# Kernel tuning notes

Measured on AMD Instinct MI355X. Metric: run time of the kernel, lower is better.

The kernel has to match this reference:

```python
import jax, jax.numpy as jnp
import numpy as np

NEG_SLOPE = 0.2  # PyG GATConv default leaky_relu slope


def add_self_loops(src, dst, ea, n_nodes):
    # PyG add_self_loops with fill_value='mean': self-loop attr = mean of
    # incoming edge attrs per destination node (0 if no incoming edges).
    cnt = jax.ops.segment_sum(jnp.ones(dst.shape, ea.dtype), dst, num_segments=n_nodes)
    mean_ea = jax.ops.segment_sum(ea, dst, num_segments=n_nodes) / jnp.maximum(cnt, 1.0)[:, None]
    loop = jnp.arange(n_nodes, dtype=src.dtype)
    return (jnp.concatenate([src, loop]),
            jnp.concatenate([dst, loop]),
            jnp.concatenate([ea, mean_ea], axis=0))


def gat_conv(x, src, dst, ea, W, att_src, att_dst, We, att_edge, bias, heads, ch, concat):
    n = x.shape[0]
    xs = (x @ W).reshape(n, heads, ch)                      # [N,H,C]
    a_src = (xs * att_src).sum(-1)                          # [N,H]
    a_dst = (xs * att_dst).sum(-1)                          # [N,H]
    ea_p = (ea @ We).reshape(-1, heads, ch)                 # [E,H,C]
    a_e = (ea_p * att_edge).sum(-1)                         # [E,H]
    logits = jax.nn.leaky_relu(a_src[src] + a_dst[dst] + a_e, NEG_SLOPE)
    m = jax.ops.segment_max(logits, dst, num_segments=n)    # segment softmax over dst
    e = jnp.exp(logits - m[dst])
    denom = jax.ops.segment_sum(e, dst, num_segments=n)
    alpha = e / (denom[dst] + 1e-16)                        # [E,H]
    out = jax.ops.segment_sum(alpha[:, :, None] * xs[src], dst, num_segments=n)  # [N,H,C]
    out = out.reshape(n, heads * ch) if concat else out.mean(axis=1)
    return out + bias


def setup_inputs() -> dict:
    key = jax.random.key(0)
    ks = jax.random.split(key, 14)
    N, E, F_IN, H, C1, C2 = 50000, 800000, 128, 2, 64, 64
    s = 0.05
    return {
        "x": jax.random.normal(ks[0], (N, F_IN), jnp.float32),
        "edge_index": jax.random.randint(ks[1], (2, E), 0, N, jnp.int32),
        "edge_weight": jax.random.uniform(ks[2], (E,), jnp.float32),
        # layer 1 (heads=2, concat=True)
        "W1": jax.random.normal(ks[3], (F_IN, H * C1), jnp.float32) * s,
        "att_src1": jax.random.normal(ks[4], (1, H, C1), jnp.float32) * s,
        "att_dst1": jax.random.normal(ks[5], (1, H, C1), jnp.float32) * s,
        "We1": jax.random.normal(ks[6], (1, H * C1), jnp.float32) * s,
        "att_edge1": jax.random.normal(ks[7], (1, H, C1), jnp.float32) * s,
        "b1": jnp.zeros((H * C1,), jnp.float32),
        # layer 2 (heads=1, concat=False)
        "W2": jax.random.normal(ks[8], (H * C1, C2), jnp.float32) * s,
        "att_src2": jax.random.normal(ks[9], (1, 1, C2), jnp.float32) * s,
        "att_dst2": jax.random.normal(ks[10], (1, 1, C2), jnp.float32) * s,
        "We2": jax.random.normal(ks[11], (1, C2), jnp.float32) * s,
        "att_edge2": jax.random.normal(ks[12], (1, 1, C2), jnp.float32) * s,
        "b2": jnp.zeros((C2,), jnp.float32),
    }


def reference(x, edge_index, edge_weight, W1, att_src1, att_dst1, We1, att_edge1, b1,
              W2, att_src2, att_dst2, We2, att_edge2, b2):
    n = x.shape[0]
    ea = edge_weight[:, None]  # edge_dim=1
    src, dst, ea = add_self_loops(edge_index[0], edge_index[1], ea, n)
    h = gat_conv(x, src, dst, ea, W1, att_src1, att_dst1, We1, att_edge1, b1,
                 heads=2, ch=64, concat=True)
    h = jax.nn.elu(h)
    out = gat_conv(h, src, dst, ea, W2, att_src2, att_dst2, We2, att_edge2, b2,
                   heads=1, ch=64, concat=False)
    return out
```

## Files before the change

### kernel.cpp

```cpp
#include <hip/hip_runtime.h>
#include <math.h>

#define NEG_SLOPE 0.2f

typedef unsigned int u32;
typedef unsigned short u16;
typedef unsigned long long u64;

typedef __attribute__((ext_vector_type(8))) short short8;
typedef __attribute__((ext_vector_type(4))) float f32x4;

__device__ __forceinline__ float bf2f(u16 h) {
  union { u32 u; float f; } c; c.u = ((u32)h) << 16; return c.f;
}
__device__ __forceinline__ u16 f2bf(float f) {
  union { float f; u32 u; } c; c.f = f;
  return (u16)((c.u + 0x7FFFu + ((c.u >> 16) & 1u)) >> 16);
}

__global__ __launch_bounds__(256) void k_hist(const int* __restrict__ dst, int E, int epb,
                                              u32* __restrict__ hist) {
  __shared__ u32 h[256];
  h[threadIdx.x] = 0;
  __syncthreads();
  int b = blockIdx.x;
  int beg = b * epb, end = beg + epb; if (end > E) end = E;
  for (int i = beg + threadIdx.x; i < end; i += 256)
    atomicAdd(&h[(u32)dst[i] >> 8], 1u);
  __syncthreads();
  hist[threadIdx.x * 256 + b] = h[threadIdx.x];
}

__global__ __launch_bounds__(256) void k_scanrow(u32* __restrict__ hist, u32* __restrict__ btot) {
  int bkt = blockIdx.x, t = threadIdx.x;
  u32 orig = hist[bkt * 256 + t];
  u32 v = orig;
  #pragma unroll
  for (int off = 1; off < 64; off <<= 1) {
    u32 u_ = __shfl_up(v, off);
    if ((t & 63) >= off) v += u_;
  }
  __shared__ u32 ws[4];
  if ((t & 63) == 63) ws[t >> 6] = v;
  __syncthreads();
  u32 add = 0; int w = t >> 6;
  if (w > 0) add += ws[0];
  if (w > 1) add += ws[1];
  if (w > 2) add += ws[2];
  u32 incl = v + add;
  hist[bkt * 256 + t] = incl - orig;
  if (t == 255) btot[bkt] = incl;
}

__global__ __launch_bounds__(256) void k_scanb(const u32* __restrict__ btot, u32* __restrict__ bstart) {
  int t = threadIdx.x;
  u32 orig = btot[t];
  u32 v = orig;
  #pragma unroll
  for (int off = 1; off < 64; off <<= 1) {
    u32 u_ = __shfl_up(v, off);
    if ((t & 63) >= off) v += u_;
  }
  __shared__ u32 ws[4];
  if ((t & 63) == 63) ws[t >> 6] = v;
  __syncthreads();
  u32 add = 0; int w = t >> 6;
  if (w > 0) add += ws[0];
  if (w > 1) add += ws[1];
  if (w > 2) add += ws[2];
  u32 incl = v + add;
  bstart[t] = incl - orig;
  if (t == 255) bstart[256] = incl;
}

__global__ __launch_bounds__(256) void k_binscatter(const int* __restrict__ src,
                                                    const int* __restrict__ dst,
                                                    const float* __restrict__ ew,
                                                    const u32* __restrict__ hist,
                                                    const u32* __restrict__ bstart,
                                                    u64* __restrict__ stage, int E, int epb) {
  __shared__ u32 cur[256];
  int b = blockIdx.x;
  cur[threadIdx.x] = bstart[threadIdx.x] + hist[threadIdx.x * 256 + b];
  __syncthreads();
  int beg = b * epb, end = beg + epb; if (end > E) end = E;
  for (int i = beg + threadIdx.x; i < end; i += 256) {
    int d = dst[i];
    u32 bkt = (u32)d >> 8;
    u32 pos = atomicAdd(&cur[bkt], 1u);
    float w = ew[i];
    u32 wq = (u32)(w * 65536.0f); if (wq > 65535u) wq = 65535u;
    stage[pos] = ((u64)((u32)d & 255u) << 32) | ((u64)wq << 16) | (u64)(u32)src[i];
  }
}

__global__ __launch_bounds__(256) void k_bucket(const u64* __restrict__ stage,
                                                const u32* __restrict__ bstart,
                                                u32* __restrict__ col,
                                                u32* __restrict__ ninfo, int n) {
  int bkt = blockIdx.x;
  int beg = (int)bstart[bkt], end = (int)bstart[bkt + 1];
  __shared__ u32 pk[256];
  pk[threadIdx.x] = 0;
  __syncthreads();
  for (int i = beg + threadIdx.x; i < end; i += 256) {
    u64 sv = stage[i];
    u32 ln = (u32)(sv >> 32) & 255u;
    u32 wq = (u32)((sv >> 16) & 0xFFFFu);
    u32 old = atomicAdd(&pk[ln], (1u << 24) | wq);
    u32 rank = old >> 24;
    if (rank < 64u)
      col[((((u32)bkt << 8) + ln) << 6) + rank] = (u32)sv;
  }
  __syncthreads();
  int v = (bkt << 8) + threadIdx.x;
  if (v < n) {
    u32 p = pk[threadIdx.x];
    u32 deg = p >> 24;
    float mean = ((float)(p & 0xFFFFFFu) * (1.0f / 65536.0f)) / (float)(deg > 1 ? deg : 1);
    u32 mq = (u32)(mean * 65536.0f); if (mq > 65535u) mq = 65535u;
    u32 dc = deg > 64u ? 64u : deg;
    ninfo[v] = (dc << 16) | mq;
  }
}

template<int H>
__global__ void k_bfrag(const float* __restrict__ W, uint4* __restrict__ bfrag) {
  int tid = blockIdx.x * 256 + threadIdx.x;
  int f = tid >> 6, lane = tid & 63;
  const int NF = H * 4 * 4 * 2;
  if (f >= NF) return;
  int p = f & 1, t = (f >> 1) & 3, cg = f >> 3;
  int colc = 16 * cg + (lane & 15);
  int k0 = 32 * t + 8 * (lane >> 4);
  u16 v[8];
  #pragma unroll
  for (int j = 0; j < 8; j++) {
    float w = W[(size_t)(k0 + j) * (H * 64) + colc];
    u32 bits = __float_as_uint(w);
    if (p == 0) v[j] = (u16)(bits >> 16);
    else        v[j] = f2bf(w - __uint_as_float(bits & 0xffff0000u));
  }
  uint4 o = { (u32)v[0] | ((u32)v[1] << 16), (u32)v[2] | ((u32)v[3] << 16),
              (u32)v[4] | ((u32)v[5] << 16), (u32)v[6] | ((u32)v[7] << 16) };
  bfrag[f * 64 + lane] = o;
}

template<int H>
__global__ __launch_bounds__(256) void k_gemm_mfma(const float* __restrict__ A,
                                                   const uint4* __restrict__ bfrag,
                                                   u16* __restrict__ xs_bf,
                                                   const float* __restrict__ att_src,
                                                   const float* __restrict__ att_dst,
                                                   float* __restrict__ a_src_out,
                                                   float* __restrict__ a_dst_out,
                                                   int nrows) {
  const int NCG = H * 4;
  int lane = threadIdx.x & 63;
  int wv = threadIdx.x >> 6;
  int lrow = lane & 15, lk = lane >> 4;
  int r0 = blockIdx.x * 64 + wv * 16;
  int arow = r0 + lrow; if (arow > nrows - 1) arow = nrows - 1;
  const float* ap = A + (size_t)arow * 128;

  f32x4 acc[NCG];
  #pragma unroll
  for (int cg = 0; cg < NCG; cg++) acc[cg] = (f32x4){0.f, 0.f, 0.f, 0.f};

  #pragma unroll
  for (int t = 0; t < 4; t++) {
    float4 av0 = *(const float4*)(ap + 32 * t + 8 * lk);
    float4 av1 = *(const float4*)(ap + 32 * t + 8 * lk + 4);
    float af[8] = {av0.x, av0.y, av0.z, av0.w, av1.x, av1.y, av1.z, av1.w};
    short8 ahi, alo;
    #pragma unroll
    for (int j = 0; j < 8; j++) {
      u32 bits = __float_as_uint(af[j]);
      ahi[j] = (short)(bits >> 16);
      alo[j] = (short)f2bf(af[j] - __uint_as_float(bits & 0xffff0000u));
    }
    #pragma unroll
    for (int cg = 0; cg < NCG; cg++) {
      union { uint4 u; short8 s; } bh, bl;
      bh.u = bfrag[((cg * 4 + t) * 2 + 0) * 64 + lane];
      bl.u = bfrag[((cg * 4 + t) * 2 + 1) * 64 + lane];
      acc[cg] = __builtin_amdgcn_mfma_f32_16x16x32_bf16(ahi, bh.s, acc[cg], 0, 0, 0);
      acc[cg] = __builtin_amdgcn_mfma_f32_16x16x32_bf16(ahi, bl.s, acc[cg], 0, 0, 0);
      acc[cg] = __builtin_amdgcn_mfma_f32_16x16x32_bf16(alo, bh.s, acc[cg], 0, 0, 0);
    }
  }

  float ps[2][4], pd[2][4];
  #pragma unroll
  for (int h = 0; h < 2; h++)
    #pragma unroll
    for (int r = 0; r < 4; r++) { ps[h][r] = 0.f; pd[h][r] = 0.f; }

  #pragma unroll
  for (int cg = 0; cg < NCG; cg++) {
    int colbase = 16 * cg + lrow;
    float asv = att_src[colbase];
    float adv = att_dst[colbase];
    const int h = (H == 2) ? (cg >> 2) : 0;
    #pragma unroll
    for (int r = 0; r < 4; r++) {
      ps[h][r] += acc[cg][r] * asv;
      pd[h][r] += acc[cg][r] * adv;
      int row = r0 + 4 * lk + r;
      if (row < nrows) xs_bf[(size_t)row * (H * 64) + colbase] = f2bf(acc[cg][r]);
    }
  }
  #pragma unroll
  for (int h = 0; h < H; h++)
    #pragma unroll
    for (int r = 0; r < 4; r++)
      #pragma unroll
      for (int off = 8; off; off >>= 1) {
        ps[h][r] += __shfl_xor(ps[h][r], off);
        pd[h][r] += __shfl_xor(pd[h][r], off);
      }
  if (lrow == 0) {
    #pragma unroll
    for (int r = 0; r < 4; r++) {
      int row = r0 + 4 * lk + r;
      if (row < nrows) {
        #pragma unroll
        for (int h = 0; h < H; h++) {
          a_src_out[row * H + h] = ps[h][r];
          a_dst_out[row * H + h] = pd[h][r];
        }
      }
    }
  }
}

__global__ void k_scalars(const float* __restrict__ We1, const float* __restrict__ ae1,
                          const float* __restrict__ We2, const float* __restrict__ ae2,
                          float* __restrict__ out) {
  int t = threadIdx.x;
  if (t == 0) { float s = 0; for (int c = 0; c < 64; c++) s += We1[c] * ae1[c]; out[0] = s; }
  if (t == 1) { float s = 0; for (int c = 0; c < 64; c++) s += We1[64 + c] * ae1[64 + c]; out[1] = s; }
  if (t == 2) { float s = 0; for (int c = 0; c < 64; c++) s += We2[c] * ae2[c]; out[2] = s; }
}

__global__ __launch_bounds__(256) void k_agg1(const u32* __restrict__ ninfo,
                                              const u32* __restrict__ col,
                                              const float2* __restrict__ a_src,
                                              const float2* __restrict__ a_dst,
                                              const float* __restrict__ scal,
                                              const u16* __restrict__ xs_bf,
                                              const float* __restrict__ b1,
                                              float* __restrict__ h_out, int n) {
  int wid = (blockIdx.x * 256 + threadIdx.x) >> 4;
  int gl = threadIdx.x & 15;
  if (wid >= n) return;
  u32 nf = ninfo[wid];
  int deg = (int)(nf >> 16);
  float mean = (float)(nf & 0xFFFFu) * (1.0f / 65536.0f);
  float2 ad = a_dst[wid];
  float2 asv_s = a_src[wid];
  float sc0 = scal[0], sc1 = scal[1];
  bool hi = gl >= 8;
  float l0s = asv_s.x + ad.x + mean * sc0;
  float l1s = asv_s.y + ad.y + mean * sc1;
  l0s = l0s > 0.f ? l0s : NEG_SLOPE * l0s;
  l1s = l1s > 0.f ? l1s : NEG_SLOPE * l1s;

  const u32* cw = col + ((u32)wid << 6);
  int nch = (deg + 15) >> 4;

  float e0a[4], e1a[4]; int sa[4];
  #pragma unroll
  for (int c = 0; c < 4; c++) {
    float l0 = -1e30f, l1 = -1e30f; int s = 0;
    if (c < nch) {
      int p = c * 16 + gl;
      bool act = p < deg;
      u32 sw = cw[act ? p : 0];
      s = (int)(sw & 0xFFFFu);
      float w = (float)(sw >> 16) * (1.0f / 65536.0f);
      float2 asv = a_src[s];
      l0 = asv.x + ad.x + w * sc0;
      l1 = asv.y + ad.y + w * sc1;
      l0 = l0 > 0.f ? l0 : NEG_SLOPE * l0;
      l1 = l1 > 0.f ? l1 : NEG_SLOPE * l1;
      if (!act) { l0 = -1e30f; l1 = -1e30f; }
    }
    sa[c] = s; e0a[c] = l0; e1a[c] = l1;
  }
  float m0 = fmaxf(fmaxf(e0a[0], e0a[1]), fmaxf(e0a[2], e0a[3]));
  float m1 = fmaxf(fmaxf(e1a[0], e1a[1]), fmaxf(e1a[2], e1a[3]));
  #pragma unroll
  for (int off = 8; off; off >>= 1) {
    m0 = fmaxf(m0, __shfl_xor(m0, off, 16));
    m1 = fmaxf(m1, __shfl_xor(m1, off, 16));
  }
  m0 = fmaxf(m0, l0s); m1 = fmaxf(m1, l1s);
  float d0 = 0.f, d1 = 0.f;
  #pragma unroll
  for (int c = 0; c < 4; c++) {
    float t0 = __expf(e0a[c] - m0);
    float t1 = __expf(e1a[c] - m1);
    e0a[c] = t0; e1a[c] = t1;
    d0 += t0; d1 += t1;
  }
  #pragma unroll
  for (int off = 8; off; off >>= 1) {
    d0 += __shfl_xor(d0, off, 16);
    d1 += __shfl_xor(d1, off, 16);
  }
  float es0 = __expf(l0s - m0), es1 = __expf(l1s - m1);
  float den = (hi ? d1 + es1 : d0 + es0);
  float esl = hi ? es1 : es0;

  float acc[8];
  {
    uint4 q = *(const uint4*)&xs_bf[(size_t)wid * 128 + 8 * gl];
    acc[0] = esl * bf2f((u16)q.x); acc[1] = esl * bf2f((u16)(q.x >> 16));
    acc[2] = esl * bf2f((u16)q.y); acc[3] = esl * bf2f((u16)(q.y >> 16));
    acc[4] = esl * bf2f((u16)q.z); acc[5] = esl * bf2f((u16)(q.z >> 16));
    acc[6] = esl * bf2f((u16)q.w); acc[7] = esl * bf2f((u16)(q.w >> 16));
  }
  #pragma unroll
  for (int c = 0; c < 4; c++) {
    if (c < nch) {
      int base = c * 16;
      int cnt = deg - base; if (cnt > 16) cnt = 16;
      int j = 0;
      for (; j + 2 <= cnt; j += 2) {
        int sj0 = __shfl(sa[c], j, 16);
        int sj1 = __shfl(sa[c], j + 1, 16);
        uint4 qa = *(const uint4*)&xs_bf[(size_t)sj0 * 128 + 8 * gl];
        uint4 qb = *(const uint4*)&xs_bf[(size_t)sj1 * 128 + 8 * gl];
        float a0 = __shfl(e0a[c], j, 16),     a1 = __shfl(e1a[c], j, 16);
        float b0 = __shfl(e0a[c], j + 1, 16), b1 = __shfl(e1a[c], j + 1, 16);
        float ala = hi ? a1 : a0;
        float alb = hi ? b1 : b0;
        acc[0] += ala * bf2f((u16)qa.x); acc[1] += ala * bf2f((u16)(qa.x >> 16));
        acc[2] += ala * bf2f((u16)qa.y); acc[3] += ala * bf2f((u16)(qa.y >> 16));
        acc[4] += ala * bf2f((u16)qa.z); acc[5] += ala * bf2f((u16)(qa.z >> 16));
        acc[6] += ala * bf2f((u16)qa.w); acc[7] += ala * bf2f((u16)(qa.w >> 16));
        acc[0] += alb * bf2f((u16)qb.x); acc[1] += alb * bf2f((u16)(qb.x >> 16));
        acc[2] += alb * bf2f((u16)qb.y); acc[3] += alb * bf2f((u16)(qb.y >> 16));
        acc[4] += alb * bf2f((u16)qb.z); acc[5] += alb * bf2f((u16)(qb.z >> 16));
        acc[6] += alb * bf2f((u16)qb.w); acc[7] += alb * bf2f((u16)(qb.w >> 16));
      }
      if (j < cnt) {
        int sj = __shfl(sa[c], j, 16);
        uint4 q = *(const uint4*)&xs_bf[(size_t)sj * 128 + 8 * gl];
        float a0 = __shfl(e0a[c], j, 16), a1 = __shfl(e1a[c], j, 16);
        float al = hi ? a1 : a0;
        acc[0] += al * bf2f((u16)q.x); acc[1] += al * bf2f((u16)(q.x >> 16));
        acc[2] += al * bf2f((u16)q.y); acc[3] += al * bf2f((u16)(q.y >> 16));
        acc[4] += al * bf2f((u16)q.z); acc[5] += al * bf2f((u16)(q.z >> 16));
        acc[6] += al * bf2f((u16)q.w); acc[7] += al * bf2f((u16)(q.w >> 16));
      }
    }
  }
  float inv = 1.f / (den + 1e-16f);
  float4 blo = *(const float4*)&b1[8 * gl];
  float4 bhi = *(const float4*)&b1[8 * gl + 4];
  float o[8];
  o[0] = acc[0] * inv + blo.x; o[1] = acc[1] * inv + blo.y;
  o[2] = acc[2] * inv + blo.z; o[3] = acc[3] * inv + blo.w;
  o[4] = acc[4] * inv + bhi.x; o[5] = acc[5] * inv + bhi.y;
  o[6] = acc[6] * inv + bhi.z; o[7] = acc[7] * inv + bhi.w;
  #pragma unroll
  for (int f = 0; f < 8; f++) o[f] = o[f] > 0.f ? o[f] : expm1f(o[f]);
  float* dst = &h_out[(size_t)wid * 128 + 8 * gl];
  *(float4*)dst = make_float4(o[0], o[1], o[2], o[3]);
  *(float4*)(dst + 4) = make_float4(o[4], o[5], o[6], o[7]);
}

__global__ __launch_bounds__(256) void k_agg2(const u32* __restrict__ ninfo,
                                              const u32* __restrict__ col,
                                              const float* __restrict__ a_src,
                                              const float* __restrict__ a_dst,
                                              const float* __restrict__ scal,
                                              const u16* __restrict__ xs_bf,
                                              const float* __restrict__ b2,
                                              float* __restrict__ out, int n) {
  int wid = (blockIdx.x * 256 + threadIdx.x) >> 3;
  int gl = threadIdx.x & 7;
  if (wid >= n) return;
  u32 nf = ninfo[wid];
  int deg = (int)(nf >> 16);
  float mean = (float)(nf & 0xFFFFu) * (1.0f / 65536.0f);
  float adv = a_dst[wid];
  float sc = scal[2];
  float ls = a_src[wid] + adv + mean * sc;
  ls = ls > 0.f ? ls : NEG_SLOPE * ls;

  const u32* cw = col + ((u32)wid << 6);
  int nch = (deg + 7) >> 3;

  float ea[8]; int sa[8];
  #pragma unroll
  for (int c = 0; c < 8; c++) {
    float l = -1e30f; int s = 0;
    if (c < nch) {
      int p = c * 8 + gl;
      bool act = p < deg;
      u32 sw = cw[act ? p : 0];
      s = (int)(sw & 0xFFFFu);
      float w = (float)(sw >> 16) * (1.0f / 65536.0f);
      l = a_src[s] + adv + w * sc;
      l = l > 0.f ? l : NEG_SLOPE * l;
      if (!act) l = -1e30f;
    }
    sa[c] = s; ea[c] = l;
  }
  float m = ls;
  #pragma unroll
  for (int c = 0; c < 8; c++) m = fmaxf(m, ea[c]);
  #pragma unroll
  for (int off = 4; off; off >>= 1) m = fmaxf(m, __shfl_xor(m, off, 8));
  float d = 0.f;
  #pragma unroll
  for (int c = 0; c < 8; c++) {
    float t = __expf(ea[c] - m);
    ea[c] = t; d += t;
  }
  #pragma unroll
  for (int off = 4; off; off >>= 1) d += __shfl_xor(d, off, 8);
  float es = __expf(ls - m);
  float den = d + es;

  float acc[8];
  {
    uint4 q = *(const uint4*)&xs_bf[(size_t)wid * 64 + 8 * gl];
    acc[0] = es * bf2f((u16)q.x); acc[1] = es * bf2f((u16)(q.x >> 16));
    acc[2] = es * bf2f((u16)q.y); acc[3] = es * bf2f((u16)(q.y >> 16));
    acc[4] = es * bf2f((u16)q.z); acc[5] = es * bf2f((u16)(q.z >> 16));
    acc[6] = es * bf2f((u16)q.w); acc[7] = es * bf2f((u16)(q.w >> 16));
  }
  #pragma unroll
  for (int c = 0; c < 8; c++) {
    if (c < nch) {
      int base = c * 8;
      int cnt = deg - base; if (cnt > 8) cnt = 8;
      int j = 0;
      for (; j + 2 <= cnt; j += 2) {
        int sj0 = __shfl(sa[c], j, 8);
        int sj1 = __shfl(sa[c], j + 1, 8);
        uint4 qa = *(const uint4*)&xs_bf[(size_t)sj0 * 64 + 8 * gl];
        uint4 qb = *(const uint4*)&xs_bf[(size_t)sj1 * 64 + 8 * gl];
        float aja = __shfl(ea[c], j, 8);
        float ajb = __shfl(ea[c], j + 1, 8);
        acc[0] += aja * bf2f((u16)qa.x); acc[1] += aja * bf2f((u16)(qa.x >> 16));
        acc[2] += aja * bf2f((u16)qa.y); acc[3] += aja * bf2f((u16)(qa.y >> 16));
        acc[4] += aja * bf2f((u16)qa.z); acc[5] += aja * bf2f((u16)(qa.z >> 16));
        acc[6] += aja * bf2f((u16)qa.w); acc[7] += aja * bf2f((u16)(qa.w >> 16));
        acc[0] += ajb * bf2f((u16)qb.x); acc[1] += ajb * bf2f((u16)(qb.x >> 16));
        acc[2] += ajb * bf2f((u16)qb.y); acc[3] += ajb * bf2f((u16)(qb.y >> 16));
        acc[4] += ajb * bf2f((u16)qb.z); acc[5] += ajb * bf2f((u16)(qb.z >> 16));
        acc[6] += ajb * bf2f((u16)qb.w); acc[7] += ajb * bf2f((u16)(qb.w >> 16));
      }
      if (j < cnt) {
        int sj = __shfl(sa[c], j, 8);
        uint4 q = *(const uint4*)&xs_bf[(size_t)sj * 64 + 8 * gl];
        float aj = __shfl(ea[c], j, 8);
        acc[0] += aj * bf2f((u16)q.x); acc[1] += aj * bf2f((u16)(q.x >> 16));
        acc[2] += aj * bf2f((u16)q.y); acc[3] += aj * bf2f((u16)(q.y >> 16));
        acc[4] += aj * bf2f((u16)q.z); acc[5] += aj * bf2f((u16)(q.z >> 16));
        acc[6] += aj * bf2f((u16)q.w); acc[7] += aj * bf2f((u16)(q.w >> 16));
      }
    }
  }
  float inv = 1.f / (den + 1e-16f);
  float4 blo = *(const float4*)&b2[8 * gl];
  float4 bhi = *(const float4*)&b2[8 * gl + 4];
  float* dst = &out[(size_t)wid * 64 + 8 * gl];
  *(float4*)dst = make_float4(acc[0] * inv + blo.x, acc[1] * inv + blo.y,
                              acc[2] * inv + blo.z, acc[3] * inv + blo.w);
  *(float4*)(dst + 4) = make_float4(acc[4] * inv + bhi.x, acc[5] * inv + bhi.y,
                                    acc[6] * inv + bhi.z, acc[7] * inv + bhi.w);
}

extern "C" void kernel_launch(void* const* d_in, const int* in_sizes, int n_in,
                              void* d_out, int out_size, void* d_ws, size_t ws_size,
                              hipStream_t stream) {
  const float* x   = (const float*)d_in[0];
  const int*   ei  = (const int*)d_in[1];
  const float* ew  = (const float*)d_in[2];
  const float* W1  = (const float*)d_in[3];
  const float* as1 = (const float*)d_in[4];
  const float* ad1 = (const float*)d_in[5];
  const float* We1 = (const float*)d_in[6];
  const float* ae1 = (const float*)d_in[7];
  const float* b1  = (const float*)d_in[8];
  const float* W2  = (const float*)d_in[9];
  const float* as2 = (const float*)d_in[10];
  const float* ad2 = (const float*)d_in[11];
  const float* We2 = (const float*)d_in[12];
  const float* ae2 = (const float*)d_in[13];
  const float* b2  = (const float*)d_in[14];

  const int n = in_sizes[0] / 128;
  const int E = in_sizes[1] / 2;
  const int epb = (E + 255) / 256;
  const int nbk = (n + 255) >> 8;

  char* wsb = (char*)d_ws;
  size_t off = 0;
  auto alloc = [&](size_t bytes) -> void* {
    void* p = wsb + off; off += (bytes + 255) & ~(size_t)255; return p;
  };
  u32*   hist    = (u32*)  alloc((size_t)256 * 256 * 4);
  u32*   btot    = (u32*)  alloc((size_t)256 * 4);
  u32*   bstart  = (u32*)  alloc((size_t)257 * 4);
  u64*   stage   = (u64*)  alloc((size_t)E * 8);
  u32*   col     = (u32*)  alloc((size_t)n * 64 * 4);
  u32*   ninfo   = (u32*)  alloc((size_t)n * 4);
  uint4* bfrag1  = (uint4*)alloc((size_t)64 * 64 * 16);
  uint4* bfrag2  = (uint4*)alloc((size_t)32 * 64 * 16);
  u16*   xs_bf   = (u16*)  alloc((size_t)n * 128 * 2);
  float* h1      = (float*)alloc((size_t)n * 128 * 4);
  float* a_src1v = (float*)alloc((size_t)n * 2 * 4);
  float* a_dst1v = (float*)alloc((size_t)n * 2 * 4);
  float* a_src2v = (float*)alloc((size_t)n * 4);
  float* a_dst2v = (float*)alloc((size_t)n * 4);
  float* scal    = (float*)alloc(64);
  if (off > ws_size) return;

  dim3 B(256);
  k_hist<<<dim3(256), B, 0, stream>>>(ei + E, E, epb, hist);
  k_scanrow<<<dim3(256), B, 0, stream>>>(hist, btot);
  k_scanb<<<dim3(1), B, 0, stream>>>(btot, bstart);
  k_binscatter<<<dim3(256), B, 0, stream>>>(ei, ei + E, ew, hist, bstart, stage, E, epb);
  k_bucket<<<dim3(nbk), B, 0, stream>>>(stage, bstart, col, ninfo, n);
  k_bfrag<2><<<dim3(16), B, 0, stream>>>(W1, bfrag1);
  k_bfrag<1><<<dim3(8), B, 0, stream>>>(W2, bfrag2);
  k_scalars<<<1, 64, 0, stream>>>(We1, ae1, We2, ae2, scal);
  k_gemm_mfma<2><<<dim3((n + 63) / 64), B, 0, stream>>>(x, bfrag1, xs_bf, as1, ad1,
                                                        a_src1v, a_dst1v, n);
  k_agg1<<<dim3((n + 15) / 16), B, 0, stream>>>(ninfo, col,
                                                (const float2*)a_src1v,
                                                (const float2*)a_dst1v,
                                                scal, xs_bf, b1, h1, n);
  k_gemm_mfma<1><<<dim3((n + 63) / 64), B, 0, stream>>>(h1, bfrag2, xs_bf, as2, ad2,
                                                        a_src2v, a_dst2v, n);
  k_agg2<<<dim3((n + 31) / 32), B, 0, stream>>>(ninfo, col, a_src2v, a_dst2v,
                                                scal, xs_bf, b2, (float*)d_out, n);
}
```

Baseline: 134.0 us.

## Fuse prep kernels and co-launch layer-1 GEMM with edge binning; pack stage to 32 bits

Merges the histogram, weight-fragment builds and scalar dot products into one prep kernel. The layer-1 MFMA GEMM and the edge bin-scatter now share a single launch, with block ranges split by role so the independent work runs concurrently. The staging buffer shrinks from 64-bit to 32-bit entries by quantising edge weights to 8 bits, which cuts scatter and bucket traffic but lowers edge-weight precision and assumes source ids fit in 16 bits. The launch count drops from about 12 to 8.

Result: faster. 120.7 us (-9.9%).

```diff
diff --git a/kernel.cpp b/kernel.cpp
--- a/kernel.cpp
+++ b/kernel.cpp
@@ -18,17 +18,53 @@
   return (u16)((c.u + 0x7FFFu + ((c.u >> 16) & 1u)) >> 16);
 }
 
-__global__ __launch_bounds__(256) void k_hist(const int* __restrict__ dst, int E, int epb,
-                                              u32* __restrict__ hist) {
-  __shared__ u32 h[256];
-  h[threadIdx.x] = 0;
-  __syncthreads();
+__device__ __forceinline__ void bfrag_build(const float* __restrict__ W, uint4* __restrict__ bfrag,
+                                            int H, int f, int lane) {
+  int p = f & 1, t = (f >> 1) & 3, cg = f >> 3;
+  int colc = 16 * cg + (lane & 15);
+  int k0 = 32 * t + 8 * (lane >> 4);
+  u16 v[8];
+  #pragma unroll
+  for (int j = 0; j < 8; j++) {
+    float w = W[(size_t)(k0 + j) * (H * 64) + colc];
+    u32 bits = __float_as_uint(w);
+    if (p == 0) v[j] = (u16)(bits >> 16);
+    else        v[j] = f2bf(w - __uint_as_float(bits & 0xffff0000u));
+  }
+  uint4 o = { (u32)v[0] | ((u32)v[1] << 16), (u32)v[2] | ((u32)v[3] << 16),
+              (u32)v[4] | ((u32)v[5] << 16), (u32)v[6] | ((u32)v[7] << 16) };
+  bfrag[f * 64 + lane] = o;
+}
+
+__global__ __launch_bounds__(256) void k_prep(const int* __restrict__ dst, int E, int epb,
+                                              u32* __restrict__ hist,
+                                              const float* __restrict__ W1, uint4* __restrict__ bfrag1,
+                                              const float* __restrict__ W2, uint4* __restrict__ bfrag2,
+                                              const float* __restrict__ We1, const float* __restrict__ ae1,
+                                              const float* __restrict__ We2, const float* __restrict__ ae2,
+                                              float* __restrict__ scal) {
   int b = blockIdx.x;
-  int beg = b * epb, end = beg + epb; if (end > E) end = E;
-  for (int i = beg + threadIdx.x; i < end; i += 256)
-    atomicAdd(&h[(u32)dst[i] >> 8], 1u);
-  __syncthreads();
-  hist[threadIdx.x * 256 + b] = h[threadIdx.x];
+  if (b < 256) {
+    __shared__ u32 h[256];
+    h[threadIdx.x] = 0;
+    __syncthreads();
+    int beg = b * epb, end = beg + epb; if (end > E) end = E;
+    for (int i = beg + threadIdx.x; i < end; i += 256)
+      atomicAdd(&h[(u32)dst[i] >> 8], 1u);
+    __syncthreads();
+    hist[threadIdx.x * 256 + b] = h[threadIdx.x];
+  } else if (b < 272) {
+    int f = (b - 256) * 4 + (threadIdx.x >> 6);
+    if (f < 64) bfrag_build(W1, bfrag1, 2, f, threadIdx.x & 63);
+  } else if (b < 280) {
+    int f = (b - 272) * 4 + (threadIdx.x >> 6);
+    if (f < 32) bfrag_build(W2, bfrag2, 1, f, threadIdx.x & 63);
+  } else {
+    int t = threadIdx.x;
+    if (t == 0) { float s = 0; for (int c = 0; c < 64; c++) s += We1[c] * ae1[c]; scal[0] = s; }
+    if (t == 1) { float s = 0; for (int c = 0; c < 64; c++) s += We1[64 + c] * ae1[64 + c]; scal[1] = s; }
+    if (t == 2) { float s = 0; for (int c = 0; c < 64; c++) s += We2[c] * ae2[c]; scal[2] = s; }
+  }
 }
 
 __global__ __launch_bounds__(256) void k_scanrow(u32* __restrict__ hist, u32* __restrict__ btot) {
@@ -73,28 +109,117 @@
   if (t == 255) bstart[256] = incl;
 }
 
-__global__ __launch_bounds__(256) void k_binscatter(const int* __restrict__ src,
-                                                    const int* __restrict__ dst,
-                                                    const float* __restrict__ ew,
-                                                    const u32* __restrict__ hist,
-                                                    const u32* __restrict__ bstart,
-                                                    u64* __restrict__ stage, int E, int epb) {
+__global__ __launch_bounds__(256) void k_gemmbin(const float* __restrict__ A,
+                                                 const uint4* __restrict__ bfrag,
+                                                 u16* __restrict__ xs_bf,
+                                                 const float* __restrict__ att_src,
+                                                 const float* __restrict__ att_dst,
+                                                 float* __restrict__ a_src_out,
+                                                 float* __restrict__ a_dst_out,
+                                                 int nrows, int nbg,
+                                                 const int* __restrict__ esrc,
+                                                 const int* __restrict__ edst,
+                                                 const float* __restrict__ ew,
+                                                 const u32* __restrict__ hist,
+                                                 const u32* __restrict__ bstart,
+                                                 u32* __restrict__ stage, int E, int epb) {
   __shared__ u32 cur[256];
-  int b = blockIdx.x;
-  cur[threadIdx.x] = bstart[threadIdx.x] + hist[threadIdx.x * 256 + b];
-  __syncthreads();
-  int beg = b * epb, end = beg + epb; if (end > E) end = E;
-  for (int i = beg + threadIdx.x; i < end; i += 256) {
-    int d = dst[i];
-    u32 bkt = (u32)d >> 8;
-    u32 pos = atomicAdd(&cur[bkt], 1u);
-    float w = ew[i];
-    u32 wq = (u32)(w * 65536.0f); if (wq > 65535u) wq = 65535u;
-    stage[pos] = ((u64)((u32)d & 255u) << 32) | ((u64)wq << 16) | (u64)(u32)src[i];
-  }
-}
-
-__global__ __launch_bounds__(256) void k_bucket(const u64* __restrict__ stage,
+  if (blockIdx.x >= nbg) {
+    int b = blockIdx.x - nbg;
+    cur[threadIdx.x] = bstart[threadIdx.x] + hist[threadIdx.x * 256 + b];
+    __syncthreads();
+    int beg = b * epb, end = beg + epb; if (end > E) end = E;
+    for (int i = beg + threadIdx.x; i < end; i += 256) {
+      int d = edst[i];
+      u32 bkt = (u32)d >> 8;
+      u32 pos = atomicAdd(&cur[bkt], 1u);
+      float w = ew[i];
+      u32 wq = (u32)(w * 256.0f); if (wq > 255u) wq = 255u;
+      stage[pos] = (((u32)d & 255u) << 24) | (wq << 16) | (u32)esrc[i];
+    }
+    return;
+  }
+  const int H = 2;
+  const int NCG = H * 4;
+  int lane = threadIdx.x & 63;
+  int wv = threadIdx.x >> 6;
+  int lrow = lane & 15, lk = lane >> 4;
+  int r0 = blockIdx.x * 64 + wv * 16;
+  int arow = r0 + lrow; if (arow > nrows - 1) arow = nrows - 1;
+  const float* ap = A + (size_t)arow * 128;
+
+  f32x4 acc[NCG];
+  #pragma unroll
+  for (int cg = 0; cg < NCG; cg++) acc[cg] = (f32x4){0.f, 0.f, 0.f, 0.f};
+
+  #pragma unroll
+  for (int t = 0; t < 4; t++) {
+    float4 av0 = *(const float4*)(ap + 32 * t + 8 * lk);
+    float4 av1 = *(const float4*)(ap + 32 * t + 8 * lk + 4);
+    float af[8] = {av0.x, av0.y, av0.z, av0.w, av1.x, av1.y, av1.z, av1.w};
+    short8 ahi, alo;
+    #pragma unroll
+    for (int j = 0; j < 8; j++) {
+      u32 bits = __float_as_uint(af[j]);
+      ahi[j] = (short)(bits >> 16);
+      alo[j] = (short)f2bf(af[j] - __uint_as_float(bits & 0xffff0000u));
+    }
+    #pragma unroll
+    for (int cg = 0; cg < NCG; cg++) {
+      union { uint4 u; short8 s; } bh, bl;
+      bh.u = bfrag[((cg * 4 + t) * 2 + 0) * 64 + lane];
+      bl.u = bfrag[((cg * 4 + t) * 2 + 1) * 64 + lane];
+      acc[cg] = __builtin_amdgcn_mfma_f32_16x16x32_bf16(ahi, bh.s, acc[cg], 0, 0, 0);
+      acc[cg] = __builtin_amdgcn_mfma_f32_16x16x32_bf16(ahi, bl.s, acc[cg], 0, 0, 0);
+      acc[cg] = __builtin_amdgcn_mfma_f32_16x16x32_bf16(alo, bh.s, acc[cg], 0, 0, 0);
+    }
+  }
+
+  float ps[2][4], pd[2][4];
+  #pragma unroll
+  for (int h = 0; h < 2; h++)
+    #pragma unroll
+    for (int r = 0; r < 4; r++) { ps[h][r] = 0.f; pd[h][r] = 0.f; }
+
+  #pragma unroll
+  for (int cg = 0; cg < NCG; cg++) {
+    int colbase = 16 * cg + lrow;
+    float asv = att_src[colbase];
+    float adv = att_dst[colbase];
+    const int h = cg >> 2;
+    #pragma unroll
+    for (int r = 0; r < 4; r++) {
+      ps[h][r] += acc[cg][r] * asv;
+      pd[h][r] += acc[cg][r] * adv;
+      int row = r0 + 4 * lk + r;
+      if (row < nrows) xs_bf[(size_t)row * (H * 64) + colbase] = f2bf(acc[cg][r]);
+    }
+  }
+  #pragma unroll
+  for (int h = 0; h < H; h++)
+    #pragma unroll
+    for (int r = 0; r < 4; r++)
+      #pragma unroll
+      for (int off = 8; off; off >>= 1) {
+        ps[h][r] += __shfl_xor(ps[h][r], off);
+        pd[h][r] += __shfl_xor(pd[h][r], off);
+      }
+  if (lrow == 0) {
+    #pragma unroll
+    for (int r = 0; r < 4; r++) {
+      int row = r0 + 4 * lk + r;
+      if (row < nrows) {
+        #pragma unroll
+        for (int h = 0; h < H; h++) {
+          a_src_out[row * H + h] = ps[h][r];
+          a_dst_out[row * H + h] = pd[h][r];
+        }
+      }
+    }
+  }
+}
+
+__global__ __launch_bounds__(256) void k_bucket(const u32* __restrict__ stage,
                                                 const u32* __restrict__ bstart,
                                                 u32* __restrict__ col,
                                                 u32* __restrict__ ninfo, int n) {
@@ -104,58 +229,35 @@
   pk[threadIdx.x] = 0;
   __syncthreads();
   for (int i = beg + threadIdx.x; i < end; i += 256) {
-    u64 sv = stage[i];
-    u32 ln = (u32)(sv >> 32) & 255u;
-    u32 wq = (u32)((sv >> 16) & 0xFFFFu);
+    u32 sv = stage[i];
+    u32 ln = sv >> 24;
+    u32 wq = (sv >> 16) & 0xFFu;
     u32 old = atomicAdd(&pk[ln], (1u << 24) | wq);
     u32 rank = old >> 24;
     if (rank < 64u)
-      col[((((u32)bkt << 8) + ln) << 6) + rank] = (u32)sv;
+      col[((((u32)bkt << 8) + ln) << 6) + rank] = sv & 0x00FFFFFFu;
   }
   __syncthreads();
   int v = (bkt << 8) + threadIdx.x;
   if (v < n) {
     u32 p = pk[threadIdx.x];
     u32 deg = p >> 24;
-    float mean = ((float)(p & 0xFFFFFFu) * (1.0f / 65536.0f)) / (float)(deg > 1 ? deg : 1);
+    float mean = ((float)(p & 0xFFFFFFu) * (1.0f / 256.0f)) / (float)(deg > 1 ? deg : 1);
     u32 mq = (u32)(mean * 65536.0f); if (mq > 65535u) mq = 65535u;
     u32 dc = deg > 64u ? 64u : deg;
     ninfo[v] = (dc << 16) | mq;
   }
 }
 
-template<int H>
-__global__ void k_bfrag(const float* __restrict__ W, uint4* __restrict__ bfrag) {
-  int tid = blockIdx.x * 256 + threadIdx.x;
-  int f = tid >> 6, lane = tid & 63;
-  const int NF = H * 4 * 4 * 2;
-  if (f >= NF) return;
-  int p = f & 1, t = (f >> 1) & 3, cg = f >> 3;
-  int colc = 16 * cg + (lane & 15);
-  int k0 = 32 * t + 8 * (lane >> 4);
-  u16 v[8];
-  #pragma unroll
-  for (int j = 0; j < 8; j++) {
-    float w = W[(size_t)(k0 + j) * (H * 64) + colc];
-    u32 bits = __float_as_uint(w);
-    if (p == 0) v[j] = (u16)(bits >> 16);
-    else        v[j] = f2bf(w - __uint_as_float(bits & 0xffff0000u));
-  }
-  uint4 o = { (u32)v[0] | ((u32)v[1] << 16), (u32)v[2] | ((u32)v[3] << 16),
-              (u32)v[4] | ((u32)v[5] << 16), (u32)v[6] | ((u32)v[7] << 16) };
-  bfrag[f * 64 + lane] = o;
-}
-
-template<int H>
-__global__ __launch_bounds__(256) void k_gemm_mfma(const float* __restrict__ A,
-                                                   const uint4* __restrict__ bfrag,
-                                                   u16* __restrict__ xs_bf,
-                                                   const float* __restrict__ att_src,
-                                                   const float* __restrict__ att_dst,
-                                                   float* __restrict__ a_src_out,
-                                                   float* __restrict__ a_dst_out,
-                                                   int nrows) {
-  const int NCG = H * 4;
+__global__ __launch_bounds__(256) void k_gemm_mfma1(const float* __restrict__ A,
+                                                    const uint4* __restrict__ bfrag,
+                                                    u16* __restrict__ xs_bf,
+                                                    const float* __restrict__ att_src,
+                                                    const float* __restrict__ att_dst,
+                                                    float* __restrict__ a_src_out,
+                                                    float* __restrict__ a_dst_out,
+                                                    int nrows) {
+  const int NCG = 4;
   int lane = threadIdx.x & 63;
   int wv = threadIdx.x >> 6;
   int lrow = lane & 15, lk = lane >> 4;
@@ -190,57 +292,40 @@
     }
   }
 
-  float ps[2][4], pd[2][4];
-  #pragma unroll
-  for (int h = 0; h < 2; h++)
-    #pragma unroll
-    for (int r = 0; r < 4; r++) { ps[h][r] = 0.f; pd[h][r] = 0.f; }
+  float ps[4], pd[4];
+  #pragma unroll
+  for (int r = 0; r < 4; r++) { ps[r] = 0.f; pd[r] = 0.f; }
 
   #pragma unroll
   for (int cg = 0; cg < NCG; cg++) {
     int colbase = 16 * cg + lrow;
     float asv = att_src[colbase];
     float adv = att_dst[colbase];
-    const int h = (H == 2) ? (cg >> 2) : 0;
     #pragma unroll
     for (int r = 0; r < 4; r++) {
-      ps[h][r] += acc[cg][r] * asv;
-      pd[h][r] += acc[cg][r] * adv;
+      ps[r] += acc[cg][r] * asv;
+      pd[r] += acc[cg][r] * adv;
       int row = r0 + 4 * lk + r;
-      if (row < nrows) xs_bf[(size_t)row * (H * 64) + colbase] = f2bf(acc[cg][r]);
-    }
-  }
-  #pragma unroll
-  for (int h = 0; h < H; h++)
-    #pragma unroll
-    for (int r = 0; r < 4; r++)
-      #pragma unroll
-      for (int off = 8; off; off >>= 1) {
-        ps[h][r] += __shfl_xor(ps[h][r], off);
-        pd[h][r] += __shfl_xor(pd[h][r], off);
-      }
+      if (row < nrows) xs_bf[(size_t)row * 64 + colbase] = f2bf(acc[cg][r]);
+    }
+  }
+  #pragma unroll
+  for (int r = 0; r < 4; r++)
+    #pragma unroll
+    for (int off = 8; off; off >>= 1) {
+      ps[r] += __shfl_xor(ps[r], off);
+      pd[r] += __shfl_xor(pd[r], off);
+    }
   if (lrow == 0) {
     #pragma unroll
     for (int r = 0; r < 4; r++) {
       int row = r0 + 4 * lk + r;
       if (row < nrows) {
-        #pragma unroll
-        for (int h = 0; h < H; h++) {
-          a_src_out[row * H + h] = ps[h][r];
-          a_dst_out[row * H + h] = pd[h][r];
-        }
+        a_src_out[row] = ps[r];
+        a_dst_out[row] = pd[r];
       }
     }
   }
-}
-
-__global__ void k_scalars(const float* __restrict__ We1, const float* __restrict__ ae1,
-                          const float* __restrict__ We2, const float* __restrict__ ae2,
-                          float* __restrict__ out) {
-  int t = threadIdx.x;
-  if (t == 0) { float s = 0; for (int c = 0; c < 64; c++) s += We1[c] * ae1[c]; out[0] = s; }
-  if (t == 1) { float s = 0; for (int c = 0; c < 64; c++) s += We1[64 + c] * ae1[64 + c]; out[1] = s; }
-  if (t == 2) { float s = 0; for (int c = 0; c < 64; c++) s += We2[c] * ae2[c]; out[2] = s; }
 }
 
 __global__ __launch_bounds__(256) void k_agg1(const u32* __restrict__ ninfo,
@@ -278,7 +363,7 @@
       bool act = p < deg;
       u32 sw = cw[act ? p : 0];
       s = (int)(sw & 0xFFFFu);
-      float w = (float)(sw >> 16) * (1.0f / 65536.0f);
+      float w = (float)(sw >> 16) * (1.0f / 256.0f);
       float2 asv = a_src[s];
       l0 = asv.x + ad.x + w * sc0;
       l1 = asv.y + ad.y + w * sc1;
@@ -403,7 +488,7 @@
       bool act = p < deg;
       u32 sw = cw[act ? p : 0];
       s = (int)(sw & 0xFFFFu);
-      float w = (float)(sw >> 16) * (1.0f / 65536.0f);
+      float w = (float)(sw >> 16) * (1.0f / 256.0f);
       l = a_src[s] + adv + w * sc;
       l = l > 0.f ? l : NEG_SLOPE * l;
       if (!act) l = -1e30f;
@@ -500,6 +585,7 @@
   const int E = in_sizes[1] / 2;
   const int epb = (E + 255) / 256;
   const int nbk = (n + 255) >> 8;
+  const int nbg = (n + 63) / 64;
 
   char* wsb = (char*)d_ws;
   size_t off = 0;
@@ -509,7 +595,7 @@
   u32*   hist    = (u32*)  alloc((size_t)256 * 256 * 4);
   u32*   btot    = (u32*)  alloc((size_t)256 * 4);
   u32*   bstart  = (u32*)  alloc((size_t)257 * 4);
-  u64*   stage   = (u64*)  alloc((size_t)E * 8);
+  u32*   stage   = (u32*)  alloc((size_t)E * 4);
   u32*   col     = (u32*)  alloc((size_t)n * 64 * 4);
   u32*   ninfo   = (u32*)  alloc((size_t)n * 4);
   uint4* bfrag1  = (uint4*)alloc((size_t)64 * 64 * 16);
@@ -524,22 +610,20 @@
   if (off > ws_size) return;
 
   dim3 B(256);
-  k_hist<<<dim3(256), B, 0, stream>>>(ei + E, E, epb, hist);
+  k_prep<<<dim3(281), B, 0, stream>>>(ei + E, E, epb, hist, W1, bfrag1, W2, bfrag2,
+                                      We1, ae1, We2, ae2, scal);
   k_scanrow<<<dim3(256), B, 0, stream>>>(hist, btot);
   k_scanb<<<dim3(1), B, 0, stream>>>(btot, bstart);
-  k_binscatter<<<dim3(256), B, 0, stream>>>(ei, ei + E, ew, hist, bstart, stage, E, epb);
+  k_gemmbin<<<dim3(nbg + 256), B, 0, stream>>>(x, bfrag1, xs_bf, as1, ad1,
+                                               a_src1v, a_dst1v, n, nbg,
+                                               ei, ei + E, ew, hist, bstart, stage, E, epb);
   k_bucket<<<dim3(nbk), B, 0, stream>>>(stage, bstart, col, ninfo, n);
-  k_bfrag<2><<<dim3(16), B, 0, stream>>>(W1, bfrag1);
-  k_bfrag<1><<<dim3(8), B, 0, stream>>>(W2, bfrag2);
-  k_scalars<<<1, 64, 0, stream>>>(We1, ae1, We2, ae2, scal);
-  k_gemm_mfma<2><<<dim3((n + 63) / 64), B, 0, stream>>>(x, bfrag1, xs_bf, as1, ad1,
-                                                        a_src1v, a_dst1v, n);
   k_agg1<<<dim3((n + 15) / 16), B, 0, stream>>>(ninfo, col,
                                                 (const float2*)a_src1v,
                                                 (const float2*)a_dst1v,
                                                 scal, xs_bf, b1, h1, n);
-  k_gemm_mfma<1><<<dim3((n + 63) / 64), B, 0, stream>>>(h1, bfrag2, xs_bf, as2, ad2,
-                                                        a_src2v, a_dst2v, n);
+  k_gemm_mfma1<<<dim3((n + 63) / 64), B, 0, stream>>>(h1, bfrag2, xs_bf, as2, ad2,
+                                                      a_src2v, a_dst2v, n);
   k_agg2<<<dim3((n + 31) / 32), B, 0, stream>>>(ninfo, col, a_src2v, a_dst2v,
                                                 scal, xs_bf, b2, (float*)d_out, n);
 }
```
